# Kernel tuning notes

Measured on AMD Instinct MI355X. Metric: run time of the kernel, lower is better.

## Reference

```python
import jax, jax.numpy as jnp
import numpy as np

N_ATOMS = 200_000
N_EDGES = 10_000_000
N_MOL = 128


def setup_inputs() -> dict:
    key = jax.random.key(0)
    k1, k2, k3, k4, k5, k6, k7 = jax.random.split(key, 7)
    dEdRij = jax.random.normal(k1, (N_EDGES, 3), dtype=jnp.float32)
    Rij = jax.random.normal(k2, (N_EDGES, 3), dtype=jnp.float32)
    R = jax.random.normal(k3, (N_ATOMS, 3), dtype=jnp.float32)
    # Non-degenerate cells: ~10 Angstrom cubic boxes with small perturbation
    cell = jnp.eye(3, dtype=jnp.float32) * 10.0 + 0.1 * jax.random.normal(k4, (N_MOL, 3, 3), dtype=jnp.float32)
    idx_i = jax.random.randint(k5, (N_EDGES,), 0, N_ATOMS, dtype=jnp.int32)
    idx_j = jax.random.randint(k6, (N_EDGES,), 0, N_ATOMS, dtype=jnp.int32)
    idx_m = jnp.sort(jax.random.randint(k7, (N_ATOMS,), 0, N_MOL, dtype=jnp.int32))
    return {"dEdRij": dEdRij, "Rij": Rij, "R": R, "cell": cell,
            "idx_i": idx_i, "idx_j": idx_j, "idx_m": idx_m}


def reference(dEdRij, Rij, R, cell, idx_i, idx_j, idx_m):
    N = R.shape[0]
    M = cell.shape[0]
    # Forces: F = sum_{edges into i} dE/dRij - sum_{edges from j} dE/dRij
    forces = jnp.zeros_like(R).at[idx_i].add(dEdRij).at[idx_j].add(-dEdRij)
    # Per-edge outer product [E,3,3]: Rij[:, :, None] * dEdRij[:, None, :]
    stress_edge = dEdRij[:, None, :] * Rij[:, :, None]
    # Scatter to atoms, then reduce atoms -> molecules
    stress_i = jnp.zeros((N, 3, 3), dtype=R.dtype).at[idx_i].add(stress_edge)
    stress = jax.ops.segment_sum(stress_i, idx_m, num_segments=M)  # [M,3,3]
    # Cell volume via scalar triple product a . (b x c)
    volume = jnp.sum(cell[:, 0, :] * jnp.cross(cell[:, 1, :], cell[:, 2, :]), axis=1)  # [M]
    stress_out = (stress / volume[:, None, None]).reshape(M * 3, 3)
    return forces, stress_out
```

## Files before the change

### kernel.cpp

```cpp
#include <hip/hip_runtime.h>
#include <hip/hip_bf16.h>

#define N_MOL 128
#define STRESS_FLOATS (N_MOL * 9)
#define APB 400
#define MAXB 512
#define EPB 2048
#define BLK 256

__global__ void zero_f32_kernel(float* __restrict__ p, size_t n) {
    size_t i = (size_t)blockIdx.x * blockDim.x + threadIdx.x;
    if (i < n) p[i] = 0.f;
}

__global__ void __launch_bounds__(256)
scatter_kernel(const float* __restrict__ dEdRij,
               const float* __restrict__ Rij,
               const int*   __restrict__ idx_i,
               const int*   __restrict__ idx_j,
               const int*   __restrict__ idx_m,
               float4* __restrict__ rec,
               int*    __restrict__ cnt,
               float*  __restrict__ spart,
               int e0_chunk, int n_edges_chunk, int B, int CAP)
{
    __shared__ int   hist[MAXB];
    __shared__ int   base[MAXB];
    __shared__ float smem[STRESS_FLOATS];

    for (int t = threadIdx.x; t < MAXB; t += blockDim.x) hist[t] = 0;
    for (int t = threadIdx.x; t < STRESS_FLOATS; t += blockDim.x) smem[t] = 0.f;
    __syncthreads();

    const int be0 = e0_chunk + blockIdx.x * EPB;
    const int be1 = min(be0 + EPB, e0_chunk + n_edges_chunk);

    for (int e = be0 + threadIdx.x; e < be1; e += blockDim.x) {
        atomicAdd(&hist[idx_i[e] / APB], 1);
        atomicAdd(&hist[idx_j[e] / APB], 1);
    }
    __syncthreads();

    for (int t = threadIdx.x; t < B; t += blockDim.x) {
        int h = hist[t];
        base[t] = h ? atomicAdd(&cnt[t], h) : 0;
        hist[t] = 0;
    }
    __syncthreads();

    for (int e = be0 + threadIdx.x; e < be1; e += blockDim.x) {
        const int i = idx_i[e];
        const int j = idx_j[e];
        const float dx = dEdRij[3*e+0], dy = dEdRij[3*e+1], dz = dEdRij[3*e+2];
        const float rx = Rij[3*e+0],    ry = Rij[3*e+1],    rz = Rij[3*e+2];

        const int m = idx_m[i];
        float* s = &smem[m * 9];
        atomicAdd(&s[0], rx * dx);
        atomicAdd(&s[1], rx * dy);
        atomicAdd(&s[2], rx * dz);
        atomicAdd(&s[3], ry * dx);
        atomicAdd(&s[4], ry * dy);
        atomicAdd(&s[5], ry * dz);
        atomicAdd(&s[6], rz * dx);
        atomicAdd(&s[7], rz * dy);
        atomicAdd(&s[8], rz * dz);

        int bi = i / APB;
        int pos = atomicAdd(&hist[bi], 1);
        int slot = base[bi] + pos;
        if (slot < CAP)
            rec[(size_t)bi * CAP + slot] =
                make_float4(__int_as_float(i), dx, dy, dz);

        int bj = j / APB;
        pos  = atomicAdd(&hist[bj], 1);
        slot = base[bj] + pos;
        if (slot < CAP)
            rec[(size_t)bj * CAP + slot] =
                make_float4(__int_as_float(j), -dx, -dy, -dz);
    }

    __syncthreads();
    float* sp = spart + (size_t)blockIdx.x * STRESS_FLOATS;
    for (int t = threadIdx.x; t < STRESS_FLOATS; t += blockDim.x)
        sp[t] += smem[t];
}

__global__ void __launch_bounds__(256)
accum_kernel(const float4* __restrict__ rec,
             const int*    __restrict__ cnt,
             float* __restrict__ forces,
             int CAP, int n3)
{
    __shared__ float facc[APB * 3];
    const int b = blockIdx.x;
    for (int t = threadIdx.x; t < APB * 3; t += blockDim.x) facc[t] = 0.f;
    __syncthreads();

    int n = cnt[b];
    if (n > CAP) n = CAP;
    const float4* rb = rec + (size_t)b * CAP;

    for (int r = threadIdx.x; r < n; r += blockDim.x) {
        float4 q = rb[r];
        int a = __float_as_int(q.x);
        int l = a - b * APB;
        atomicAdd(&facc[l * 3 + 0], q.y);
        atomicAdd(&facc[l * 3 + 1], q.z);
        atomicAdd(&facc[l * 3 + 2], q.w);
    }
    __syncthreads();

    const int o = b * APB * 3;
    for (int t = threadIdx.x; t < APB * 3; t += blockDim.x) {
        int a3 = o + t;
        if (a3 < n3) forces[a3] += facc[t];
    }
}

__global__ void reduce_stress_kernel(const float* __restrict__ spart,
                                     const float* __restrict__ cell,
                                     float* __restrict__ out_stress,
                                     int rows)
{
    int t = blockIdx.x * blockDim.x + threadIdx.x;
    if (t >= STRESS_FLOATS) return;
    float acc = 0.f;
    #pragma unroll 8
    for (int b = 0; b < rows; ++b)
        acc += spart[(size_t)b * STRESS_FLOATS + t];
    const int m = t / 9;
    const float* c = &cell[m * 9];
    const float a0 = c[0], a1 = c[1], a2 = c[2];
    const float b0 = c[3], b1 = c[4], b2 = c[5];
    const float c0 = c[6], c1 = c[7], c2 = c[8];
    const float x0 = b1 * c2 - b2 * c1;
    const float x1 = b2 * c0 - b0 * c2;
    const float x2 = b0 * c1 - b1 * c0;
    const float vol = a0 * x0 + a1 * x1 + a2 * x2;
    out_stress[t] = acc / vol;
}

__global__ void zero_f64_kernel(double* __restrict__ p, int n) {
    int i = blockIdx.x * blockDim.x + threadIdx.x;
    if (i < n) p[i] = 0.0;
}

__global__ void __launch_bounds__(256)
edge_kernel_f64(const float* __restrict__ dEdRij,
                const float* __restrict__ Rij,
                const int*   __restrict__ idx_i,
                const int*   __restrict__ idx_j,
                const int*   __restrict__ idx_m,
                double* __restrict__ facc,
                float*  __restrict__ spart,
                int E)
{
    __shared__ float smem[STRESS_FLOATS];
    for (int t = threadIdx.x; t < STRESS_FLOATS; t += blockDim.x) smem[t] = 0.f;
    __syncthreads();
    const int stride = gridDim.x * blockDim.x;
    for (int e = blockIdx.x * blockDim.x + threadIdx.x; e < E; e += stride) {
        const int i = idx_i[e], j = idx_j[e];
        const float dx = dEdRij[3*e+0], dy = dEdRij[3*e+1], dz = dEdRij[3*e+2];
        const float rx = Rij[3*e+0],    ry = Rij[3*e+1],    rz = Rij[3*e+2];
        double* fi = facc + 3 * (size_t)i;
        unsafeAtomicAdd(fi + 0, (double) dx);
        unsafeAtomicAdd(fi + 1, (double) dy);
        unsafeAtomicAdd(fi + 2, (double) dz);
        double* fj = facc + 3 * (size_t)j;
        unsafeAtomicAdd(fj + 0, (double)-dx);
        unsafeAtomicAdd(fj + 1, (double)-dy);
        unsafeAtomicAdd(fj + 2, (double)-dz);
        const int m = idx_m[i];
        float* s = &smem[m * 9];
        atomicAdd(&s[0], rx*dx); atomicAdd(&s[1], rx*dy); atomicAdd(&s[2], rx*dz);
        atomicAdd(&s[3], ry*dx); atomicAdd(&s[4], ry*dy); atomicAdd(&s[5], ry*dz);
        atomicAdd(&s[6], rz*dx); atomicAdd(&s[7], rz*dy); atomicAdd(&s[8], rz*dz);
    }
    __syncthreads();
    float* sp = spart + (size_t)blockIdx.x * STRESS_FLOATS;
    for (int t = threadIdx.x; t < STRESS_FLOATS; t += blockDim.x) sp[t] = smem[t];
}

__global__ void reduce_forces_f64_kernel(const double* __restrict__ facc,
                                         float* __restrict__ forces, int n3)
{
    int t = blockIdx.x * blockDim.x + threadIdx.x;
    if (t < n3) forces[t] = (float)facc[t];
}

__global__ void reduce_stress_rows_kernel(const float* __restrict__ spart,
                                          const float* __restrict__ cell,
                                          float* __restrict__ out_stress,
                                          int rows)
{
    int t = blockIdx.x * blockDim.x + threadIdx.x;
    if (t >= STRESS_FLOATS) return;
    float acc = 0.f;
    for (int b = 0; b < rows; ++b)
        acc += spart[(size_t)b * STRESS_FLOATS + t];
    const int m = t / 9;
    const float* c = &cell[m * 9];
    const float a0 = c[0], a1 = c[1], a2 = c[2];
    const float b0 = c[3], b1 = c[4], b2 = c[5];
    const float c0 = c[6], c1 = c[7], c2 = c[8];
    const float x0 = b1*c2 - b2*c1, x1 = b2*c0 - b0*c2, x2 = b0*c1 - b1*c0;
    const float vol = a0*x0 + a1*x1 + a2*x2;
    out_stress[t] = acc / vol;
}

extern "C" void kernel_launch(void* const* d_in, const int* in_sizes, int n_in,
                              void* d_out, int out_size, void* d_ws, size_t ws_size,
                              hipStream_t stream)
{
    const float* dEdRij = (const float*)d_in[0];
    const float* Rij    = (const float*)d_in[1];
    const float* R      = (const float*)d_in[2];  (void)R;
    const float* cell   = (const float*)d_in[3];
    const int*   idx_i  = (const int*)d_in[4];
    const int*   idx_j  = (const int*)d_in[5];
    const int*   idx_m  = (const int*)d_in[6];

    const int E  = in_sizes[0] / 3;
    const int N  = in_sizes[2] / 3;
    const int n3 = N * 3;

    float* out        = (float*)d_out;
    float* forces     = out;
    float* stress_out = out + (size_t)n3;

    const int B = (N + APB - 1) / APB;

    int nchunks = 0, CAP = 0, ROWS = 0;
    size_t rec_f4 = 0, spart_f = 0;
    if (B <= MAXB) {
        const int cand[9] = {5, 8, 10, 12, 15, 20, 25, 30, 40};
        for (int ci = 0; ci < 9; ++ci) {
            int nc   = cand[ci];
            int CH   = (E + nc - 1) / nc;
            int cap  = (3 * CH) / B + 64;
            int rows = (CH + EPB - 1) / EPB;
            size_t need = (size_t)B * cap * sizeof(float4)
                        + (size_t)rows * STRESS_FLOATS * sizeof(float)
                        + (size_t)nc * B * sizeof(int) + 256;
            if (need <= ws_size) {
                nchunks = nc; CAP = cap; ROWS = rows;
                rec_f4  = (size_t)B * cap;
                spart_f = (size_t)rows * STRESS_FLOATS;
                break;
            }
        }
    }

    if (nchunks > 0) {
        float4* rec   = (float4*)d_ws;
        float*  spart = (float*)(rec + rec_f4);
        int*    cnt   = (int*)(spart + spart_f);

        const size_t zf = spart_f + (size_t)nchunks * B;
        zero_f32_kernel<<<(int)((zf + BLK - 1) / BLK), BLK, 0, stream>>>(
            spart, zf);
        zero_f32_kernel<<<(n3 + BLK - 1) / BLK, BLK, 0, stream>>>(
            forces, (size_t)n3);

        const int CH = (E + nchunks - 1) / nchunks;
        int chunk = 0;
        for (int s = 0; s < E; s += CH, ++chunk) {
            const int ce = min(CH, E - s);
            const int nb = (ce + EPB - 1) / EPB;

            scatter_kernel<<<nb, BLK, 0, stream>>>(
                dEdRij, Rij, idx_i, idx_j, idx_m,
                rec, cnt + (size_t)chunk * B, spart, s, ce, B, CAP);

            accum_kernel<<<B, BLK, 0, stream>>>(
                rec, cnt + (size_t)chunk * B, forces, CAP, n3);
        }

        reduce_stress_kernel<<<(STRESS_FLOATS + BLK - 1) / BLK, BLK, 0, stream>>>(
            spart, cell, stress_out, ROWS);
    } else {
        double* facc   = (double*)d_ws;
        float*  spartf = (float*)(facc + n3);

        zero_f64_kernel<<<(n3 + BLK - 1) / BLK, BLK, 0, stream>>>(facc, n3);
        edge_kernel_f64<<<2048, BLK, 0, stream>>>(
            dEdRij, Rij, idx_i, idx_j, idx_m, facc, spartf, E);
        reduce_forces_f64_kernel<<<(n3 + BLK - 1) / BLK, BLK, 0, stream>>>(
            facc, forces, n3);
        reduce_stress_rows_kernel<<<(STRESS_FLOATS + BLK - 1) / BLK, BLK, 0, stream>>>(
            spartf, cell, stress_out, 2048);
    }
}
```

Baseline: 1.175 ms.

## Stage binned force records in LDS and write them out coalesced

The scatter kernel now keeps its edge indices in registers between the histogram pass and the scatter pass, so idx_i and idx_j are read only once. It prefix-scans the per-bin histogram, stages each block's records in shared memory sorted by bin, and writes them to global memory in contiguous runs instead of as random per-edge stores. The accumulate kernel unrolls its loads by four to keep more loads in flight, and the chunk candidates now allow fewer, larger chunks. The 64KB float4 staging buffer raises LDS use per block, which lowers occupancy, and the scan adds extra barriers.

```diff
diff --git a/kernel.cpp b/kernel.cpp
--- a/kernel.cpp
+++ b/kernel.cpp
@@ -24,9 +24,12 @@
                float*  __restrict__ spart,
                int e0_chunk, int n_edges_chunk, int B, int CAP)
 {
-    __shared__ int   hist[MAXB];
-    __shared__ int   base[MAXB];
-    __shared__ float smem[STRESS_FLOATS];
+    __shared__ int    hist[MAXB];
+    __shared__ int    scan[MAXB];
+    __shared__ int    cur[MAXB];
+    __shared__ int    shiftb[MAXB];
+    __shared__ float  smem[STRESS_FLOATS];
+    __shared__ float4 stg[EPB * 2];
 
     for (int t = threadIdx.x; t < MAXB; t += blockDim.x) hist[t] = 0;
     for (int t = threadIdx.x; t < STRESS_FLOATS; t += blockDim.x) smem[t] = 0.f;
@@ -35,22 +38,46 @@
     const int be0 = e0_chunk + blockIdx.x * EPB;
     const int be1 = min(be0 + EPB, e0_chunk + n_edges_chunk);
 
-    for (int e = be0 + threadIdx.x; e < be1; e += blockDim.x) {
-        atomicAdd(&hist[idx_i[e] / APB], 1);
-        atomicAdd(&hist[idx_j[e] / APB], 1);
-    }
-    __syncthreads();
+    int ei[8], ej[8];
+    #pragma unroll
+    for (int k = 0; k < 8; ++k) {
+        const int e = be0 + k * BLK + threadIdx.x;
+        ei[k] = -1; ej[k] = -1;
+        if (e < be1) {
+            ei[k] = idx_i[e];
+            ej[k] = idx_j[e];
+            atomicAdd(&hist[ei[k] / APB], 1);
+            atomicAdd(&hist[ej[k] / APB], 1);
+        }
+    }
+    __syncthreads();
+    for (int t = threadIdx.x; t < MAXB; t += blockDim.x) scan[t] = hist[t];
+    __syncthreads();
+
+    for (int off = 1; off < MAXB; off <<= 1) {
+        const int a = threadIdx.x, b2 = threadIdx.x + BLK;
+        const int v0 = (a  >= off) ? scan[a  - off] : 0;
+        const int v1 = (b2 >= off) ? scan[b2 - off] : 0;
+        __syncthreads();
+        scan[a]  += v0;
+        scan[b2] += v1;
+        __syncthreads();
+    }
 
     for (int t = threadIdx.x; t < B; t += blockDim.x) {
-        int h = hist[t];
-        base[t] = h ? atomicAdd(&cnt[t], h) : 0;
-        hist[t] = 0;
-    }
-    __syncthreads();
-
-    for (int e = be0 + threadIdx.x; e < be1; e += blockDim.x) {
-        const int i = idx_i[e];
-        const int j = idx_j[e];
+        const int h    = hist[t];
+        const int excl = scan[t] - h;
+        const int g    = h ? atomicAdd(&cnt[t], h) : 0;
+        cur[t]    = excl;
+        shiftb[t] = t * CAP + g - excl;
+    }
+    __syncthreads();
+
+    #pragma unroll
+    for (int k = 0; k < 8; ++k) {
+        const int e = be0 + k * BLK + threadIdx.x;
+        if (e >= be1) continue;
+        const int i = ei[k], j = ej[k];
         const float dx = dEdRij[3*e+0], dy = dEdRij[3*e+1], dz = dEdRij[3*e+2];
         const float rx = Rij[3*e+0],    ry = Rij[3*e+1],    rz = Rij[3*e+2];
 
@@ -66,19 +93,21 @@
         atomicAdd(&s[7], rz * dy);
         atomicAdd(&s[8], rz * dz);
 
-        int bi = i / APB;
-        int pos = atomicAdd(&hist[bi], 1);
-        int slot = base[bi] + pos;
-        if (slot < CAP)
-            rec[(size_t)bi * CAP + slot] =
-                make_float4(__int_as_float(i), dx, dy, dz);
-
-        int bj = j / APB;
-        pos  = atomicAdd(&hist[bj], 1);
-        slot = base[bj] + pos;
-        if (slot < CAP)
-            rec[(size_t)bj * CAP + slot] =
-                make_float4(__int_as_float(j), -dx, -dy, -dz);
+        int p = atomicAdd(&cur[i / APB], 1);
+        stg[p] = make_float4(__int_as_float(i), dx, dy, dz);
+        p = atomicAdd(&cur[j / APB], 1);
+        stg[p] = make_float4(__int_as_float(j), -dx, -dy, -dz);
+    }
+    __syncthreads();
+
+    const int total = 2 * (be1 - be0);
+    for (int t = threadIdx.x; t < total; t += blockDim.x) {
+        const float4 q = stg[t];
+        const int a = __float_as_int(q.x);
+        const int b = a / APB;
+        const int gidx = t + shiftb[b];
+        if (gidx < (b + 1) * CAP)
+            rec[gidx] = q;
     }
 
     __syncthreads();
@@ -101,20 +130,34 @@
     int n = cnt[b];
     if (n > CAP) n = CAP;
     const float4* rb = rec + (size_t)b * CAP;
-
-    for (int r = threadIdx.x; r < n; r += blockDim.x) {
-        float4 q = rb[r];
-        int a = __float_as_int(q.x);
-        int l = a - b * APB;
-        atomicAdd(&facc[l * 3 + 0], q.y);
-        atomicAdd(&facc[l * 3 + 1], q.z);
-        atomicAdd(&facc[l * 3 + 2], q.w);
-    }
-    __syncthreads();
-
-    const int o = b * APB * 3;
+    const int abase = b * APB;
+
+#define ACC(q)                                             \
+    {                                                      \
+        const int l = __float_as_int((q).x) - abase;       \
+        atomicAdd(&facc[l * 3 + 0], (q).y);                \
+        atomicAdd(&facc[l * 3 + 1], (q).z);                \
+        atomicAdd(&facc[l * 3 + 2], (q).w);                \
+    }
+
+    int r = threadIdx.x;
+    for (; r + 3 * BLK < n; r += 4 * BLK) {
+        const float4 q0 = rb[r];
+        const float4 q1 = rb[r + BLK];
+        const float4 q2 = rb[r + 2 * BLK];
+        const float4 q3 = rb[r + 3 * BLK];
+        ACC(q0); ACC(q1); ACC(q2); ACC(q3);
+    }
+    for (; r < n; r += BLK) {
+        const float4 q = rb[r];
+        ACC(q);
+    }
+#undef ACC
+
+    __syncthreads();
+    const int o = abase * 3;
     for (int t = threadIdx.x; t < APB * 3; t += blockDim.x) {
-        int a3 = o + t;
+        const int a3 = o + t;
         if (a3 < n3) forces[a3] += facc[t];
     }
 }
@@ -236,8 +279,8 @@
     int nchunks = 0, CAP = 0, ROWS = 0;
     size_t rec_f4 = 0, spart_f = 0;
     if (B <= MAXB) {
-        const int cand[9] = {5, 8, 10, 12, 15, 20, 25, 30, 40};
-        for (int ci = 0; ci < 9; ++ci) {
+        const int cand[10] = {3, 4, 5, 8, 10, 12, 15, 20, 25, 40};
+        for (int ci = 0; ci < 10; ++ci) {
             int nc   = cand[ci];
             int CH   = (E + nc - 1) / nc;
             int cap  = (3 * CH) / B + 64;
```

After: 1.202 ms. 1.02x slower.
